# Kernel tuning notes

Hardware: AMD Instinct MI355X
Metric: run time of the kernel (lower is better)

Reference implementation:

```python
import jax, jax.numpy as jnp
import numpy as np

Q, C, T, D_IN, D_H = 512, 512, 128, 512, 256


def setup_inputs() -> dict:
    key = jax.random.key(0)
    ks = jax.random.split(key, 8)
    s_in = 1.0 / np.sqrt(D_IN)
    s_h = 1.0 / np.sqrt(D_H)
    return {
        "audio": jax.random.normal(ks[0], (Q, T, D_IN), jnp.float32),
        "video": jax.random.normal(ks[1], (C, T, D_IN), jnp.float32),
        "a_w1": jax.random.normal(ks[2], (D_IN, D_H), jnp.float32) * s_in,
        "a_b1": jnp.zeros((D_H,), jnp.float32),
        "a_w2": jax.random.normal(ks[3], (D_H, D_H), jnp.float32) * s_h,
        "a_b2": jnp.zeros((D_H,), jnp.float32),
        "v_w1": jax.random.normal(ks[4], (D_IN, D_H), jnp.float32) * s_in,
        "v_b1": jnp.zeros((D_H,), jnp.float32),
        "v_w2": jax.random.normal(ks[5], (D_H, D_H), jnp.float32) * s_h,
        "v_b2": jnp.zeros((D_H,), jnp.float32),
        "W": jax.random.normal(ks[6], (D_H, D_H), jnp.float32) * s_h,
        "max_lag": 4,
    }


def _mlp(x, w1, b1, w2, b2):
    # Linear -> ReLU -> Linear
    h = jnp.maximum(x @ w1 + b1, 0.0)
    return h @ w2 + b2


def reference(audio, video, a_w1, a_b1, a_w2, a_b2,
              v_w1, v_b1, v_w2, v_b2, W, max_lag):
    a = _mlp(audio, a_w1, a_b1, a_w2, a_b2)   # [Q, T, D_H]
    v = _mlp(video, v_w1, v_b1, v_w2, v_b2)   # [C, T, D_H]
    # roll along time commutes with the per-frame linear map, so project once
    pv = jnp.einsum('ctd,df->ctf', v, W)      # [C, T, D_H]
    best = None
    for delta in range(-max_lag, max_lag + 1):
        shifted = jnp.roll(pv, delta, axis=1)
        score = jnp.einsum('qtd,ctd->qc', a, shifted)  # [Q, C]
        best = score if best is None else jnp.maximum(best, score)
    return best
```

## Files before the change

### kernel.cpp

```cpp
#include <hip/hip_runtime.h>
#include <cstdint>
#include <cstddef>

typedef __attribute__((ext_vector_type(8))) short frag8;
typedef __attribute__((ext_vector_type(4))) float f32x4;

static __device__ __forceinline__ unsigned short f2bf_r(float f) {
    return (unsigned short)((__float_as_uint(f) + 0x8000u) >> 16);
}

static __device__ __forceinline__ void gll16(const void* g, void* l) {
    __builtin_amdgcn_global_load_lds(
        (const __attribute__((address_space(1))) unsigned int*)g,
        (__attribute__((address_space(3))) unsigned int*)l, 16, 0, 0);
}

__global__ __launch_bounds__(256, 2)
void mlp_fused(const float* __restrict__ X0, const float* __restrict__ X1,
               const unsigned short* __restrict__ W1T0, const unsigned short* __restrict__ W1T1,
               const float* __restrict__ b1v0, const float* __restrict__ b1v1,
               const unsigned short* __restrict__ W2T0, const unsigned short* __restrict__ W2T1,
               const float* __restrict__ b2v0, const float* __restrict__ b2v1,
               unsigned short* __restrict__ O0, unsigned short* __restrict__ O1)
{
    __shared__ __align__(16) unsigned short As[64 * 72];
    __shared__ __align__(16) unsigned short Bs[256 * 64];
    __shared__ __align__(16) unsigned short hs[64 * 264];

    const int mod = blockIdx.y;
    const float* X = mod ? X1 : X0;
    const unsigned short* W1T = mod ? W1T1 : W1T0;
    const unsigned short* W2T = mod ? W2T1 : W2T0;
    const float* b1 = mod ? b1v1 : b1v0;
    const float* b2 = mod ? b2v1 : b2v0;
    unsigned short* O = mod ? O1 : O0;

    const int t    = threadIdx.x;
    const int wave = t >> 6;
    const int lane = t & 63;
    const int quad = lane >> 4;
    const int l15  = lane & 15;
    const int m0   = blockIdx.x * 64;

    const int rowB = lane >> 3;
    const int qB   = (lane & 7) ^ rowB;
    const int nRowBase = wave * 64 + rowB;
    unsigned short* BsW = Bs + wave * 4096;
    const int swz = l15 & 7;

    const int sRow = t >> 4;
    const int sCol = (t & 15) * 4;

    f32x4 acc[4][4];
    #pragma unroll
    for (int i = 0; i < 4; ++i)
        #pragma unroll
        for (int j = 0; j < 4; ++j)
            acc[i][j] = (f32x4){0.f, 0.f, 0.f, 0.f};

    float4 xr[4];
    #pragma unroll
    for (int p = 0; p < 4; ++p)
        xr[p] = *(const float4*)(X + (size_t)(m0 + p * 16 + sRow) * 512 + sCol);

    for (int k0 = 0; k0 < 512; k0 += 64) {
        #pragma unroll
        for (int p = 0; p < 4; ++p) {
            const float4 v = xr[p];
            const unsigned int a0 = __float_as_uint(v.x) + 0x8000u;
            const unsigned int a1 = __float_as_uint(v.y) + 0x8000u;
            const unsigned int a2 = __float_as_uint(v.z) + 0x8000u;
            const unsigned int a3 = __float_as_uint(v.w) + 0x8000u;
            uint2 pk;
            pk.x = __builtin_amdgcn_perm(a1, a0, 0x07060302u);
            pk.y = __builtin_amdgcn_perm(a3, a2, 0x07060302u);
            *(uint2*)&As[(p * 16 + sRow) * 72 + sCol] = pk;
        }
        #pragma unroll
        for (int p = 0; p < 8; ++p)
            gll16(W1T + (size_t)(nRowBase + p * 8) * 512 + qB * 8 + k0, BsW + p * 512);
        __syncthreads();

        if (k0 + 64 < 512) {
            #pragma unroll
            for (int p = 0; p < 4; ++p)
                xr[p] = *(const float4*)(X + (size_t)(m0 + p * 16 + sRow) * 512 + (k0 + 64) + sCol);
        }

        frag8 af[2][4], bf[2][4];
        #pragma unroll
        for (int i = 0; i < 4; ++i)
            #pragma unroll
            for (int kh = 0; kh < 2; ++kh)
                af[kh][i] = *(const frag8*)&As[(i * 16 + l15) * 72 + kh * 32 + quad * 8];
        #pragma unroll
        for (int j = 0; j < 4; ++j) {
            const int row = wave * 64 + j * 16 + l15;
            #pragma unroll
            for (int kh = 0; kh < 2; ++kh)
                bf[kh][j] = *(const frag8*)&Bs[row * 64 + (((kh * 4 + quad) ^ swz) * 8)];
        }
        __builtin_amdgcn_s_setprio(1);
        #pragma unroll
        for (int kh = 0; kh < 2; ++kh)
            #pragma unroll
            for (int i = 0; i < 4; ++i)
                #pragma unroll
                for (int j = 0; j < 4; ++j)
                    acc[i][j] = __builtin_amdgcn_mfma_f32_16x16x32_bf16(af[kh][i], bf[kh][j], acc[i][j], 0, 0, 0);
        __builtin_amdgcn_s_setprio(0);
        __syncthreads();
    }

    #pragma unroll
    for (int j = 0; j < 4; ++j) {
        const int col = wave * 64 + j * 16 + l15;
        const float bv = b1[col];
        #pragma unroll
        for (int i = 0; i < 4; ++i) {
            const int rl = i * 16 + quad * 4;
            #pragma unroll
            for (int r = 0; r < 4; ++r)
                hs[(rl + r) * 264 + col] = f2bf_r(fmaxf(acc[i][j][r] + bv, 0.0f));
        }
    }
    __syncthreads();

    #pragma unroll
    for (int i = 0; i < 4; ++i)
        #pragma unroll
        for (int j = 0; j < 4; ++j)
            acc[i][j] = (f32x4){0.f, 0.f, 0.f, 0.f};

    for (int k0 = 0; k0 < 256; k0 += 64) {
        #pragma unroll
        for (int p = 0; p < 8; ++p)
            gll16(W2T + (size_t)(nRowBase + p * 8) * 256 + qB * 8 + k0, BsW + p * 512);
        __syncthreads();

        frag8 af[2][4], bf[2][4];
        #pragma unroll
        for (int i = 0; i < 4; ++i)
            #pragma unroll
            for (int kh = 0; kh < 2; ++kh)
                af[kh][i] = *(const frag8*)&hs[(i * 16 + l15) * 264 + k0 + kh * 32 + quad * 8];
        #pragma unroll
        for (int j = 0; j < 4; ++j) {
            const int row = wave * 64 + j * 16 + l15;
            #pragma unroll
            for (int kh = 0; kh < 2; ++kh)
                bf[kh][j] = *(const frag8*)&Bs[row * 64 + (((kh * 4 + quad) ^ swz) * 8)];
        }
        __builtin_amdgcn_s_setprio(1);
        #pragma unroll
        for (int kh = 0; kh < 2; ++kh)
            #pragma unroll
            for (int i = 0; i < 4; ++i)
                #pragma unroll
                for (int j = 0; j < 4; ++j)
                    acc[i][j] = __builtin_amdgcn_mfma_f32_16x16x32_bf16(af[kh][i], bf[kh][j], acc[i][j], 0, 0, 0);
        __builtin_amdgcn_s_setprio(0);
        __syncthreads();
    }

    #pragma unroll
    for (int j = 0; j < 4; ++j) {
        const int col = wave * 64 + j * 16 + l15;
        const float bv = b2[col];
        #pragma unroll
        for (int i = 0; i < 4; ++i) {
            const int rl = i * 16 + quad * 4;
            #pragma unroll
            for (int r = 0; r < 4; ++r)
                hs[(rl + r) * 264 + col] = f2bf_r(acc[i][j][r] + bv);
        }
    }
    __syncthreads();
    #pragma unroll
    for (int u = 0; u < 8; ++u) {
        const int chunk = u * 256 + t;
        const int row = chunk >> 5;
        const int c16 = (chunk & 31) * 8;
        uint4 v = *(const uint4*)&hs[row * 264 + c16];
        *(uint4*)&O[(size_t)(m0 + row) * 256 + c16] = v;
    }
}

__global__ __launch_bounds__(512, 2)
void gemm_corr(const unsigned short* __restrict__ A, const unsigned short* __restrict__ B,
               float* __restrict__ partial, int sc)
{
    __shared__ __align__(16) unsigned short lds[4 * 2 * 8192];

    const int t    = threadIdx.x;
    const int wave = t >> 6;
    const int lane = t & 63;
    const int quad = lane >> 4;
    const int l15  = lane & 15;
    const int wr   = wave >> 2;
    const int wc   = wave & 3;

    const int L = blockIdx.x + (blockIdx.y << 1) + (blockIdx.z << 2);
    int ell;
    if (sc == 7) {
        const int xcd = L & 7, off = L >> 3;
        ell = (xcd < 4 ? xcd * 32 : 128 + (xcd - 4) * 31) + off;
    } else {
        const int xcd = L & 7, off = L >> 3;
        ell = xcd * 18 + off;
    }
    const int bx   = ell & 1;
    const int by   = (ell >> 1) & 1;
    const int rest = ell >> 2;
    const int d    = rest % 9;
    const int s    = rest / 9;
    const int m0   = by * 256;
    const int n0   = bx * 256;

    int t0, nT;
    if (sc == 7) { nT = (s == 6) ? 136 : 148; t0 = s * 148; }
    else         { nT = 256;                  t0 = s << 8; }
    const int zp     = d * sc + s;
    const int delta  = d - 4;
    const int kStart = t0 * 32;
    const int koff   = (32768 - 256 * delta) & 32767;

    const int gsrc      = (lane & 7) ^ ((lane >> 3) & 7);
    const int srcRowOff = ((lane >> 3) << 1) + (gsrc >> 2);
    const int srcCol    = (gsrc & 3) << 3;
    const size_t aSrcBase = (size_t)(m0 + srcRowOff) * 32768 + srcCol;
    const size_t bSrcBase = (size_t)(n0 + srcRowOff) * 32768 + srcCol;

    const int gphys = (((l15 & 1) << 2) | quad) ^ ((l15 >> 1) & 7);
    const int aOff  = (wr * 64 + (l15 >> 1)) * 64 + gphys * 8;
    const int bOff  = (wc * 32 + (l15 >> 1)) * 64 + gphys * 8;

    f32x4 acc[8][4];
    #pragma unroll
    for (int i = 0; i < 8; ++i)
        #pragma unroll
        for (int j = 0; j < 4; ++j)
            acc[i][j] = (f32x4){0.f, 0.f, 0.f, 0.f};

    #pragma unroll
    for (int pt = 0; pt < 3; ++pt) {
        const int kk = (kStart + pt * 32) & 32767;
        const int kb = (kk + koff) & 32767;
        #pragma unroll
        for (int qq = 0; qq < 2; ++qq) {
            const int c = wave * 2 + qq;
            gll16(A + aSrcBase + (size_t)c * 16 * 32768 + kk, &lds[pt * 16384 + c * 512]);
            gll16(B + bSrcBase + (size_t)c * 16 * 32768 + kb, &lds[pt * 16384 + 8192 + c * 512]);
        }
    }

    for (int kt0 = 0; kt0 < nT; kt0 += 4) {
        #pragma unroll
        for (int u = 0; u < 4; ++u) {
            {
                const int kk = (kStart + (kt0 + u + 3) * 32) & 32767;
                const int kb = (kk + koff) & 32767;
                unsigned short* LSa = &lds[((u + 3) & 3) * 16384 + wave * 1024];
                unsigned short* LSb = LSa + 8192;
                #pragma unroll
                for (int qq = 0; qq < 2; ++qq) {
                    const int c = wave * 2 + qq;
                    gll16(A + aSrcBase + (size_t)c * 16 * 32768 + kk, LSa + qq * 512);
                    gll16(B + bSrcBase + (size_t)c * 16 * 32768 + kb, LSb + qq * 512);
                }
            }
            asm volatile("s_waitcnt vmcnt(12)" ::: "memory");
            __builtin_amdgcn_s_barrier();
            asm volatile("" ::: "memory");

            const unsigned short* LA = &lds[u * 16384];
            const unsigned short* LB = LA + 8192;
            frag8 af[8], bf[4];
            #pragma unroll
            for (int j = 0; j < 4; ++j) bf[j] = *(const frag8*)(LB + bOff + j * 512);
            #pragma unroll
            for (int i = 0; i < 4; ++i) af[i] = *(const frag8*)(LA + aOff + i * 512);
            __builtin_amdgcn_s_setprio(1);
            #pragma unroll
            for (int i = 0; i < 4; ++i)
                #pragma unroll
                for (int j = 0; j < 4; ++j)
                    acc[i][j] = __builtin_amdgcn_mfma_f32_16x16x32_bf16(af[i], bf[j], acc[i][j], 0, 0, 0);
            __builtin_amdgcn_s_setprio(0);
            #pragma unroll
            for (int i = 4; i < 8; ++i) af[i] = *(const frag8*)(LA + aOff + i * 512);
            __builtin_amdgcn_s_setprio(1);
            #pragma unroll
            for (int i = 4; i < 8; ++i)
                #pragma unroll
                for (int j = 0; j < 4; ++j)
                    acc[i][j] = __builtin_amdgcn_mfma_f32_16x16x32_bf16(af[i], bf[j], acc[i][j], 0, 0, 0);
            __builtin_amdgcn_s_setprio(0);
            asm volatile("" ::: "memory");
            __builtin_amdgcn_s_barrier();
        }
    }
    asm volatile("s_waitcnt vmcnt(0)" ::: "memory");

    float* C = partial + ((size_t)zp << 18);
    #pragma unroll
    for (int i = 0; i < 8; ++i) {
        const int rg = m0 + wr * 128 + i * 16 + quad * 4;
        #pragma unroll
        for (int j = 0; j < 4; ++j) {
            const int cg = n0 + wc * 64 + j * 16 + l15;
            #pragma unroll
            for (int r = 0; r < 4; ++r)
                C[(size_t)(rg + r) * 512 + cg] = acc[i][j][r];
        }
    }
}

__global__ void prep(const float* __restrict__ a_w1, const float* __restrict__ v_w1,
                     const float* __restrict__ a_w2, const float* __restrict__ v_w2,
                     const float* __restrict__ W, const float* __restrict__ v_b2,
                     unsigned short* __restrict__ aw1T, unsigned short* __restrict__ vw1T,
                     unsigned short* __restrict__ aw2T,
                     unsigned short* __restrict__ WcT, float* __restrict__ bc)
{
    const int b = blockIdx.x;
    __shared__ float tl[32][33];
    __shared__ float wcol[256];
    if (b < 320) {
        const float* src; unsigned short* dst; int R, C, tile;
        if (b < 128)      { src = a_w1; dst = aw1T; R = 512; C = 256; tile = b; }
        else if (b < 256) { src = v_w1; dst = vw1T; R = 512; C = 256; tile = b - 128; }
        else              { src = a_w2; dst = aw2T; R = 256; C = 256; tile = b - 256; }
        const int tilesX = C / 32;
        const int bx = (tile % tilesX) * 32, by = (tile / tilesX) * 32;
        const int tx = threadIdx.x & 31, ty = threadIdx.x >> 5;
        #pragma unroll
        for (int r = ty; r < 32; r += 8)
            tl[r][tx] = src[(size_t)(by + r) * C + bx + tx];
        __syncthreads();
        #pragma unroll
        for (int c = ty; c < 32; c += 8)
            dst[(size_t)(bx + c) * R + by + tx] = f2bf_r(tl[tx][c]);
    } else {
        const int n = b - 320, k = threadIdx.x;
        wcol[k] = W[(size_t)k * 256 + n];
        __syncthreads();
        float s = 0.f;
        #pragma unroll 8
        for (int d = 0; d < 256; ++d) s += v_w2[(size_t)k * 256 + d] * wcol[d];
        WcT[(size_t)n * 256 + k] = f2bf_r(s);
        if (k == 0) {
            float tt = 0.f;
            for (int d = 0; d < 256; ++d) tt += v_b2[d] * wcol[d];
            bc[n] = tt;
        }
    }
}

__global__ void reduce_max(const float* __restrict__ partial, float* __restrict__ out, int sc) {
    const int idx = blockIdx.x * blockDim.x + threadIdx.x;
    float best = -3.4e38f;
    for (int d = 0; d < 9; ++d) {
        float ssum = 0.f;
        const float* p = partial + ((size_t)(d * sc) << 18) + idx;
        for (int k = 0; k < sc; ++k) ssum += p[(size_t)k << 18];
        best = fmaxf(best, ssum);
    }
    out[idx] = best;
}

extern "C" void kernel_launch(void* const* d_in, const int* in_sizes, int n_in,
                              void* d_out, int out_size, void* d_ws, size_t ws_size,
                              hipStream_t stream) {
    const float* audio = (const float*)d_in[0];
    const float* video = (const float*)d_in[1];
    const float* a_w1  = (const float*)d_in[2];
    const float* a_b1  = (const float*)d_in[3];
    const float* a_w2  = (const float*)d_in[4];
    const float* a_b2  = (const float*)d_in[5];
    const float* v_w1  = (const float*)d_in[6];
    const float* v_b1  = (const float*)d_in[7];
    const float* v_w2  = (const float*)d_in[8];
    const float* v_b2  = (const float*)d_in[9];
    const float* Wm    = (const float*)d_in[10];

    char* ws = (char*)d_ws;
    unsigned short* aw1T = (unsigned short*)(ws + 0);
    unsigned short* vw1T = (unsigned short*)(ws + 262144);
    unsigned short* aw2T = (unsigned short*)(ws + 524288);
    unsigned short* WcT  = (unsigned short*)(ws + 655360);
    float*          bc   = (float*)(ws + 786432);
    unsigned short* a_bf = (unsigned short*)(ws + 1048576);
    unsigned short* pv   = (unsigned short*)(ws + 34603008);
    float* partial       = (float*)(ws + 68157440);
    float* out = (float*)d_out;

    const int sc = (ws_size >= 134217728ull) ? 7 : 4;

    prep<<<dim3(576), 256, 0, stream>>>(a_w1, v_w1, a_w2, v_w2, Wm, v_b2,
                                        aw1T, vw1T, aw2T, WcT, bc);
    mlp_fused<<<dim3(1024, 2), 256, 0, stream>>>(
        audio, video, aw1T, vw1T, a_b1, v_b1, aw2T, WcT, a_b2, bc, a_bf, pv);
    gemm_corr<<<dim3(2, 2, 9 * sc), 512, 0, stream>>>(a_bf, pv, partial, sc);
    reduce_max<<<dim3(1024), 256, 0, stream>>>(partial, out, sc);
}
```

Before: 513.3 us.

## Add 14-way split-K correlation GEMM variant with double-buffered LDS and higher occupancy

Adds gemm_corr_hi, which splits the K (time×feature) reduction into 14 slices per lag instead of 7. It uses a 2-stage LDS buffer instead of 4 so that 4 blocks of 512 threads can be resident per CU, giving 504 blocks to fill the machine. In the MLP kernel the register-prefetched X loads are replaced with direct per-iteration loads, and the s_setprio hints are removed. The new path doubles the partial-result traffic for reduce_max and reduces MLP load/compute overlap, and it only runs when the workspace is large enough.

```diff
diff --git a/kernel.cpp b/kernel.cpp
--- a/kernel.cpp
+++ b/kernel.cpp
@@ -48,9 +48,6 @@
     unsigned short* BsW = Bs + wave * 4096;
     const int swz = l15 & 7;
 
-    const int sRow = t >> 4;
-    const int sCol = (t & 15) * 4;
-
     f32x4 acc[4][4];
     #pragma unroll
     for (int i = 0; i < 4; ++i)
@@ -58,15 +55,13 @@
         for (int j = 0; j < 4; ++j)
             acc[i][j] = (f32x4){0.f, 0.f, 0.f, 0.f};
 
-    float4 xr[4];
-    #pragma unroll
-    for (int p = 0; p < 4; ++p)
-        xr[p] = *(const float4*)(X + (size_t)(m0 + p * 16 + sRow) * 512 + sCol);
-
     for (int k0 = 0; k0 < 512; k0 += 64) {
         #pragma unroll
         for (int p = 0; p < 4; ++p) {
-            const float4 v = xr[p];
+            const int idx = p * 256 + t;
+            const int row = idx >> 4;
+            const int col = (idx & 15) * 4;
+            const float4 v = *(const float4*)(X + (size_t)(m0 + row) * 512 + k0 + col);
             const unsigned int a0 = __float_as_uint(v.x) + 0x8000u;
             const unsigned int a1 = __float_as_uint(v.y) + 0x8000u;
             const unsigned int a2 = __float_as_uint(v.z) + 0x8000u;
@@ -74,19 +69,13 @@
             uint2 pk;
             pk.x = __builtin_amdgcn_perm(a1, a0, 0x07060302u);
             pk.y = __builtin_amdgcn_perm(a3, a2, 0x07060302u);
-            *(uint2*)&As[(p * 16 + sRow) * 72 + sCol] = pk;
+            *(uint2*)&As[row * 72 + col] = pk;
         }
         #pragma unroll
         for (int p = 0; p < 8; ++p)
             gll16(W1T + (size_t)(nRowBase + p * 8) * 512 + qB * 8 + k0, BsW + p * 512);
         __syncthreads();
 
-        if (k0 + 64 < 512) {
-            #pragma unroll
-            for (int p = 0; p < 4; ++p)
-                xr[p] = *(const float4*)(X + (size_t)(m0 + p * 16 + sRow) * 512 + (k0 + 64) + sCol);
-        }
-
         frag8 af[2][4], bf[2][4];
         #pragma unroll
         for (int i = 0; i < 4; ++i)
@@ -100,7 +89,6 @@
             for (int kh = 0; kh < 2; ++kh)
                 bf[kh][j] = *(const frag8*)&Bs[row * 64 + (((kh * 4 + quad) ^ swz) * 8)];
         }
-        __builtin_amdgcn_s_setprio(1);
         #pragma unroll
         for (int kh = 0; kh < 2; ++kh)
             #pragma unroll
@@ -108,7 +96,6 @@
                 #pragma unroll
                 for (int j = 0; j < 4; ++j)
                     acc[i][j] = __builtin_amdgcn_mfma_f32_16x16x32_bf16(af[kh][i], bf[kh][j], acc[i][j], 0, 0, 0);
-        __builtin_amdgcn_s_setprio(0);
         __syncthreads();
     }
 
@@ -151,7 +138,6 @@
             for (int kh = 0; kh < 2; ++kh)
                 bf[kh][j] = *(const frag8*)&Bs[row * 64 + (((kh * 4 + quad) ^ swz) * 8)];
         }
-        __builtin_amdgcn_s_setprio(1);
         #pragma unroll
         for (int kh = 0; kh < 2; ++kh)
             #pragma unroll
@@ -159,7 +145,6 @@
                 #pragma unroll
                 for (int j = 0; j < 4; ++j)
                     acc[i][j] = __builtin_amdgcn_mfma_f32_16x16x32_bf16(af[kh][i], bf[kh][j], acc[i][j], 0, 0, 0);
-        __builtin_amdgcn_s_setprio(0);
         __syncthreads();
     }
 
@@ -185,6 +170,7 @@
         *(uint4*)&O[(size_t)(m0 + row) * 256 + c16] = v;
     }
 }
+
 
 __global__ __launch_bounds__(512, 2)
 void gemm_corr(const unsigned short* __restrict__ A, const unsigned short* __restrict__ B,
@@ -270,6 +256,127 @@
                 }
             }
             asm volatile("s_waitcnt vmcnt(12)" ::: "memory");
+            __builtin_amdgcn_s_barrier();
+            asm volatile("" ::: "memory");
+
+            const unsigned short* LA = &lds[u * 16384];
+            const unsigned short* LB = LA + 8192;
+            frag8 af[8], bf[4];
+            #pragma unroll
+            for (int j = 0; j < 4; ++j) bf[j] = *(const frag8*)(LB + bOff + j * 512);
+            #pragma unroll
+            for (int i = 0; i < 4; ++i) af[i] = *(const frag8*)(LA + aOff + i * 512);
+            __builtin_amdgcn_s_setprio(1);
+            #pragma unroll
+            for (int i = 0; i < 4; ++i)
+                #pragma unroll
+                for (int j = 0; j < 4; ++j)
+                    acc[i][j] = __builtin_amdgcn_mfma_f32_16x16x32_bf16(af[i], bf[j], acc[i][j], 0, 0, 0);
+            __builtin_amdgcn_s_setprio(0);
+            #pragma unroll
+            for (int i = 4; i < 8; ++i) af[i] = *(const frag8*)(LA + aOff + i * 512);
+            __builtin_amdgcn_s_setprio(1);
+            #pragma unroll
+            for (int i = 4; i < 8; ++i)
+                #pragma unroll
+                for (int j = 0; j < 4; ++j)
+                    acc[i][j] = __builtin_amdgcn_mfma_f32_16x16x32_bf16(af[i], bf[j], acc[i][j], 0, 0, 0);
+            __builtin_amdgcn_s_setprio(0);
+            asm volatile("" ::: "memory");
+            __builtin_amdgcn_s_barrier();
+        }
+    }
+    asm volatile("s_waitcnt vmcnt(0)" ::: "memory");
+
+    float* C = partial + ((size_t)zp << 18);
+    #pragma unroll
+    for (int i = 0; i < 8; ++i) {
+        const int rg = m0 + wr * 128 + i * 16 + quad * 4;
+        #pragma unroll
+        for (int j = 0; j < 4; ++j) {
+            const int cg = n0 + wc * 64 + j * 16 + l15;
+            #pragma unroll
+            for (int r = 0; r < 4; ++r)
+                C[(size_t)(rg + r) * 512 + cg] = acc[i][j][r];
+        }
+    }
+}
+
+__global__ __launch_bounds__(512, 4)
+void gemm_corr_hi(const unsigned short* __restrict__ A, const unsigned short* __restrict__ B,
+                  float* __restrict__ partial)
+{
+    __shared__ __align__(16) unsigned short lds[2 * 2 * 8192];
+
+    const int t    = threadIdx.x;
+    const int wave = t >> 6;
+    const int lane = t & 63;
+    const int quad = lane >> 4;
+    const int l15  = lane & 15;
+    const int wr   = wave >> 2;
+    const int wc   = wave & 3;
+
+    const int L   = blockIdx.x + (blockIdx.y << 1) + (blockIdx.z << 2);
+    const int ell = (L & 7) * 63 + (L >> 3);
+    const int bx   = ell & 1;
+    const int by   = (ell >> 1) & 1;
+    const int rest = ell >> 2;
+    const int d    = rest % 9;
+    const int s    = rest / 9;
+    const int m0   = by * 256;
+    const int n0   = bx * 256;
+
+    const int nT = (s == 13) ? 62 : 74;
+    const int t0 = s * 74;
+    const int zp     = d * 14 + s;
+    const int delta  = d - 4;
+    const int kStart = t0 * 32;
+    const int koff   = (32768 - 256 * delta) & 32767;
+
+    const int gsrc      = (lane & 7) ^ ((lane >> 3) & 7);
+    const int srcRowOff = ((lane >> 3) << 1) + (gsrc >> 2);
+    const int srcCol    = (gsrc & 3) << 3;
+    const size_t aSrcBase = (size_t)(m0 + srcRowOff) * 32768 + srcCol;
+    const size_t bSrcBase = (size_t)(n0 + srcRowOff) * 32768 + srcCol;
+
+    const int gphys = (((l15 & 1) << 2) | quad) ^ ((l15 >> 1) & 7);
+    const int aOff  = (wr * 64 + (l15 >> 1)) * 64 + gphys * 8;
+    const int bOff  = (wc * 32 + (l15 >> 1)) * 64 + gphys * 8;
+
+    f32x4 acc[8][4];
+    #pragma unroll
+    for (int i = 0; i < 8; ++i)
+        #pragma unroll
+        for (int j = 0; j < 4; ++j)
+            acc[i][j] = (f32x4){0.f, 0.f, 0.f, 0.f};
+
+    {
+        const int kk = kStart & 32767;
+        const int kb = (kk + koff) & 32767;
+        #pragma unroll
+        for (int qq = 0; qq < 2; ++qq) {
+            const int c = wave * 2 + qq;
+            gll16(A + aSrcBase + (size_t)c * 16 * 32768 + kk, &lds[c * 512]);
+            gll16(B + bSrcBase + (size_t)c * 16 * 32768 + kb, &lds[8192 + c * 512]);
+        }
+    }
+
+    for (int kt0 = 0; kt0 < nT; kt0 += 2) {
+        #pragma unroll
+        for (int u = 0; u < 2; ++u) {
+            {
+                const int kk = (kStart + (kt0 + u + 1) * 32) & 32767;
+                const int kb = (kk + koff) & 32767;
+                unsigned short* LSa = &lds[((u + 1) & 1) * 16384 + wave * 1024];
+                unsigned short* LSb = LSa + 8192;
+                #pragma unroll
+                for (int qq = 0; qq < 2; ++qq) {
+                    const int c = wave * 2 + qq;
+                    gll16(A + aSrcBase + (size_t)c * 16 * 32768 + kk, LSa + qq * 512);
+                    gll16(B + bSrcBase + (size_t)c * 16 * 32768 + kb, LSb + qq * 512);
+                }
+            }
+            asm volatile("s_waitcnt vmcnt(4)" ::: "memory");
             __builtin_amdgcn_s_barrier();
             asm volatile("" ::: "memory");
 
@@ -395,12 +502,16 @@
     float* partial       = (float*)(ws + 68157440);
     float* out = (float*)d_out;
 
-    const int sc = (ws_size >= 134217728ull) ? 7 : 4;
+    const int sc_hi_ok = (ws_size >= 68157440ull + 126ull * 1048576ull);
+    const int sc = sc_hi_ok ? 14 : ((ws_size >= 134217728ull) ? 7 : 4);
 
     prep<<<dim3(576), 256, 0, stream>>>(a_w1, v_w1, a_w2, v_w2, Wm, v_b2,
                                         aw1T, vw1T, aw2T, WcT, bc);
     mlp_fused<<<dim3(1024, 2), 256, 0, stream>>>(
         audio, video, aw1T, vw1T, a_b1, v_b1, aw2T, WcT, a_b2, bc, a_bf, pv);
-    gemm_corr<<<dim3(2, 2, 9 * sc), 512, 0, stream>>>(a_bf, pv, partial, sc);
+    if (sc == 14)
+        gemm_corr_hi<<<dim3(2, 2, 126), 512, 0, stream>>>(a_bf, pv, partial);
+    else
+        gemm_corr<<<dim3(2, 2, 9 * sc), 512, 0, stream>>>(a_bf, pv, partial, sc);
     reduce_max<<<dim3(1024), 256, 0, stream>>>(partial, out, sc);
 }
```

Result: slower. 1.805 ms (+251.7%).

## Prefetch next B fragments in main GEMM and simplify MLP X loads

Applied to the files above, without the earlier changes.

In the large split-K GEMM kernel, B fragments for the next k-step are now loaded into a register double buffer during the current step, and the vmcnt wait is tightened to make that stage resident earlier. The goal is to hide LDS read latency ahead of the MFMA chains. In the MLP kernel, the register prefetch of X is replaced with direct loads inside the loop and the s_setprio hints are removed. That shortens register lifetimes but exposes global load latency in the MLP. The tighter wait in the GEMM cuts pipeline depth, so loads have less time to land.

```diff
diff --git a/kernel.cpp b/kernel.cpp
--- a/kernel.cpp
+++ b/kernel.cpp
@@ -48,9 +48,6 @@
     unsigned short* BsW = Bs + wave * 4096;
     const int swz = l15 & 7;
 
-    const int sRow = t >> 4;
-    const int sCol = (t & 15) * 4;
-
     f32x4 acc[4][4];
     #pragma unroll
     for (int i = 0; i < 4; ++i)
@@ -58,15 +55,13 @@
         for (int j = 0; j < 4; ++j)
             acc[i][j] = (f32x4){0.f, 0.f, 0.f, 0.f};
 
-    float4 xr[4];
-    #pragma unroll
-    for (int p = 0; p < 4; ++p)
-        xr[p] = *(const float4*)(X + (size_t)(m0 + p * 16 + sRow) * 512 + sCol);
-
     for (int k0 = 0; k0 < 512; k0 += 64) {
         #pragma unroll
         for (int p = 0; p < 4; ++p) {
-            const float4 v = xr[p];
+            const int idx = p * 256 + t;
+            const int row = idx >> 4;
+            const int col = (idx & 15) * 4;
+            const float4 v = *(const float4*)(X + (size_t)(m0 + row) * 512 + k0 + col);
             const unsigned int a0 = __float_as_uint(v.x) + 0x8000u;
             const unsigned int a1 = __float_as_uint(v.y) + 0x8000u;
             const unsigned int a2 = __float_as_uint(v.z) + 0x8000u;
@@ -74,19 +69,13 @@
             uint2 pk;
             pk.x = __builtin_amdgcn_perm(a1, a0, 0x07060302u);
             pk.y = __builtin_amdgcn_perm(a3, a2, 0x07060302u);
-            *(uint2*)&As[(p * 16 + sRow) * 72 + sCol] = pk;
+            *(uint2*)&As[row * 72 + col] = pk;
         }
         #pragma unroll
         for (int p = 0; p < 8; ++p)
             gll16(W1T + (size_t)(nRowBase + p * 8) * 512 + qB * 8 + k0, BsW + p * 512);
         __syncthreads();
 
-        if (k0 + 64 < 512) {
-            #pragma unroll
-            for (int p = 0; p < 4; ++p)
-                xr[p] = *(const float4*)(X + (size_t)(m0 + p * 16 + sRow) * 512 + (k0 + 64) + sCol);
-        }
-
         frag8 af[2][4], bf[2][4];
         #pragma unroll
         for (int i = 0; i < 4; ++i)
@@ -100,7 +89,6 @@
             for (int kh = 0; kh < 2; ++kh)
                 bf[kh][j] = *(const frag8*)&Bs[row * 64 + (((kh * 4 + quad) ^ swz) * 8)];
         }
-        __builtin_amdgcn_s_setprio(1);
         #pragma unroll
         for (int kh = 0; kh < 2; ++kh)
             #pragma unroll
@@ -108,7 +96,6 @@
                 #pragma unroll
                 for (int j = 0; j < 4; ++j)
                     acc[i][j] = __builtin_amdgcn_mfma_f32_16x16x32_bf16(af[kh][i], bf[kh][j], acc[i][j], 0, 0, 0);
-        __builtin_amdgcn_s_setprio(0);
         __syncthreads();
     }
 
@@ -151,7 +138,6 @@
             for (int kh = 0; kh < 2; ++kh)
                 bf[kh][j] = *(const frag8*)&Bs[row * 64 + (((kh * 4 + quad) ^ swz) * 8)];
         }
-        __builtin_amdgcn_s_setprio(1);
         #pragma unroll
         for (int kh = 0; kh < 2; ++kh)
             #pragma unroll
@@ -159,7 +145,6 @@
                 #pragma unroll
                 for (int j = 0; j < 4; ++j)
                     acc[i][j] = __builtin_amdgcn_mfma_f32_16x16x32_bf16(af[kh][i], bf[kh][j], acc[i][j], 0, 0, 0);
-        __builtin_amdgcn_s_setprio(0);
         __syncthreads();
     }
 
@@ -242,6 +227,8 @@
         for (int j = 0; j < 4; ++j)
             acc[i][j] = (f32x4){0.f, 0.f, 0.f, 0.f};
 
+    frag8 bfb[2][4];
+
     #pragma unroll
     for (int pt = 0; pt < 3; ++pt) {
         const int kk = (kStart + pt * 32) & 32767;
@@ -253,6 +240,12 @@
             gll16(B + bSrcBase + (size_t)c * 16 * 32768 + kb, &lds[pt * 16384 + 8192 + c * 512]);
         }
     }
+    asm volatile("s_waitcnt vmcnt(8)" ::: "memory");
+    __builtin_amdgcn_s_barrier();
+    asm volatile("" ::: "memory");
+    #pragma unroll
+    for (int j = 0; j < 4; ++j)
+        bfb[0][j] = *(const frag8*)(&lds[8192] + bOff + j * 512);
 
     for (int kt0 = 0; kt0 < nT; kt0 += 4) {
         #pragma unroll
@@ -269,15 +262,13 @@
                     gll16(B + bSrcBase + (size_t)c * 16 * 32768 + kb, LSb + qq * 512);
                 }
             }
-            asm volatile("s_waitcnt vmcnt(12)" ::: "memory");
+            asm volatile("s_waitcnt vmcnt(8)" ::: "memory");
             __builtin_amdgcn_s_barrier();
             asm volatile("" ::: "memory");
 
-            const unsigned short* LA = &lds[u * 16384];
-            const unsigned short* LB = LA + 8192;
-            frag8 af[8], bf[4];
-            #pragma unroll
-            for (int j = 0; j < 4; ++j) bf[j] = *(const frag8*)(LB + bOff + j * 512);
+            const unsigned short* LA  = &lds[u * 16384];
+            const unsigned short* LBn = &lds[((u + 1) & 3) * 16384 + 8192];
+            frag8 af[8];
             #pragma unroll
             for (int i = 0; i < 4; ++i) af[i] = *(const frag8*)(LA + aOff + i * 512);
             __builtin_amdgcn_s_setprio(1);
@@ -285,16 +276,19 @@
             for (int i = 0; i < 4; ++i)
                 #pragma unroll
                 for (int j = 0; j < 4; ++j)
-                    acc[i][j] = __builtin_amdgcn_mfma_f32_16x16x32_bf16(af[i], bf[j], acc[i][j], 0, 0, 0);
+                    acc[i][j] = __builtin_amdgcn_mfma_f32_16x16x32_bf16(af[i], bfb[u & 1][j], acc[i][j], 0, 0, 0);
             __builtin_amdgcn_s_setprio(0);
             #pragma unroll
             for (int i = 4; i < 8; ++i) af[i] = *(const frag8*)(LA + aOff + i * 512);
+            #pragma unroll
+            for (int j = 0; j < 4; ++j)
+                bfb[(u + 1) & 1][j] = *(const frag8*)(LBn + bOff + j * 512);
             __builtin_amdgcn_s_setprio(1);
             #pragma unroll
             for (int i = 4; i < 8; ++i)
                 #pragma unroll
                 for (int j = 0; j < 4; ++j)
-                    acc[i][j] = __builtin_amdgcn_mfma_f32_16x16x32_bf16(af[i], bf[j], acc[i][j], 0, 0, 0);
+                    acc[i][j] = __builtin_amdgcn_mfma_f32_16x16x32_bf16(af[i], bfb[u & 1][j], acc[i][j], 0, 0, 0);
             __builtin_amdgcn_s_setprio(0);
             asm volatile("" ::: "memory");
             __builtin_amdgcn_s_barrier();
```

Result: faster. 485.3 us (median of 4 runs) (-5.5%).
